# Kernel optimization log

Measured on AMD Instinct MI355X. Metric: run time of the kernel, lower is better.

Reference implementation:

```python
import jax, jax.numpy as jnp
import numpy as np

N_NODES = 100000
N_EDGES = 3200000
N_GRAPHS = 5000
IN_DIM = 11 + 3  # QM9 num_features + pos
HID = 64


def setup_inputs() -> dict:
    key = jax.random.key(0)
    ks = jax.random.split(key, 12)
    x = jax.random.normal(ks[0], (N_NODES, 11), dtype=jnp.float32)
    pos = jax.random.normal(ks[1], (N_NODES, 3), dtype=jnp.float32)
    edge_index = jax.random.randint(ks[2], (2, N_EDGES), 0, N_NODES, dtype=jnp.int32)
    batch = jnp.sort(jax.random.randint(ks[3], (N_NODES,), 0, N_GRAPHS, dtype=jnp.int32))
    s1 = 1.0 / np.sqrt(IN_DIM)
    s2 = 1.0 / np.sqrt(HID)
    return {
        'x': x,
        'pos': pos,
        'edge_index': edge_index,
        'batch': batch,
        'W1_l': jax.random.uniform(ks[4], (IN_DIM, HID), jnp.float32, -s1, s1),
        'W1_r': jax.random.uniform(ks[5], (IN_DIM, HID), jnp.float32, -s1, s1),
        'b1': jax.random.uniform(ks[6], (HID,), jnp.float32, -s1, s1),
        'W2_l': jax.random.uniform(ks[7], (HID, HID), jnp.float32, -s2, s2),
        'W2_r': jax.random.uniform(ks[8], (HID, HID), jnp.float32, -s2, s2),
        'b2': jax.random.uniform(ks[9], (HID,), jnp.float32, -s2, s2),
        'W_lin': jax.random.uniform(ks[10], (HID, 1), jnp.float32, -s2, s2),
        'b_lin': jax.random.uniform(ks[11], (1,), jnp.float32, -s2, s2),
    }


def _sage_conv(h, src, dst, W_l, W_r, b):
    # mean-aggregate source features at target nodes (PyG SAGEConv default)
    msg = h[src]  # [E, D] gather
    agg = jax.ops.segment_sum(msg, dst, num_segments=N_NODES)
    deg = jax.ops.segment_sum(jnp.ones((src.shape[0],), h.dtype), dst, num_segments=N_NODES)
    agg = agg / jnp.maximum(deg, 1.0)[:, None]
    return agg @ W_l + h @ W_r + b


def reference(x, pos, edge_index, batch, W1_l, W1_r, b1, W2_l, W2_r, b2, W_lin, b_lin):
    h = jnp.concatenate([x, pos], axis=1)  # [N, 14]
    src, dst = edge_index[0], edge_index[1]
    h = jax.nn.relu(_sage_conv(h, src, dst, W1_l, W1_r, b1))
    h = jax.nn.relu(_sage_conv(h, src, dst, W2_l, W2_r, b2))
    # global mean pool over graphs
    pooled = jax.ops.segment_sum(h, batch, num_segments=N_GRAPHS)
    cnt = jax.ops.segment_sum(jnp.ones((N_NODES,), h.dtype), batch, num_segments=N_GRAPHS)
    pooled = pooled / jnp.maximum(cnt, 1.0)[:, None]
    return pooled @ W_lin + b_lin  # [G, 1]
```

## Files before the change

kernel.cpp:

```cpp
#include <hip/hip_runtime.h>

#define IND 14
#define INDP 16
#define HIDD 64
#define RB 512
#define NB_MAX 256
#define BH_BLOCKS 512
#define CAP 18432

typedef unsigned int uint;
typedef unsigned short ushort;

__device__ __forceinline__ float bf16lo(uint u) { return __uint_as_float(u << 16); }
__device__ __forceinline__ float bf16hi(uint u) { return __uint_as_float(u & 0xFFFF0000u); }
__device__ __forceinline__ ushort f2bf(float f) {
    uint u = __float_as_uint(f);
    u += 0x7FFFu + ((u >> 16) & 1u);
    return (ushort)(u >> 16);
}

__global__ void build_h0p(const float* __restrict__ x, const float* __restrict__ pos,
                          float* __restrict__ h0p, ushort* __restrict__ h0h, int N) {
    int tid = blockIdx.x * blockDim.x + threadIdx.x;
    int total = N * INDP;
    if (tid >= total) return;
    int n = tid >> 4, d = tid & 15;
    float v = 0.0f;
    if (d < 11) v = x[n * 11 + d];
    else if (d < 14) v = pos[n * 3 + (d - 11)];
    h0p[tid] = v;
    h0h[tid] = f2bf(v);
}

__global__ __launch_bounds__(256) void bscat_fused(const int* __restrict__ ei,
                                                   int* __restrict__ gcur,
                                                   uint* __restrict__ pairs,
                                                   int E, int NB, int chunk) {
    __shared__ int cntS[NB_MAX];
    __shared__ int baseS[NB_MAX];
    cntS[threadIdx.x] = 0;
    __syncthreads();
    int start = blockIdx.x * chunk;
    int end = min(start + chunk, E);
    for (int e = start + threadIdx.x; e < end; e += 256)
        atomicAdd(&cntS[ei[E + e] >> 9], 1);
    __syncthreads();
    if (threadIdx.x < NB) {
        int c = cntS[threadIdx.x];
        baseS[threadIdx.x] = c ? atomicAdd(&gcur[threadIdx.x], c) : 0;
        cntS[threadIdx.x] = 0;
    }
    __syncthreads();
    for (int e = start + threadIdx.x; e < end; e += 256) {
        int s = ei[e], d = ei[E + e];
        int b = d >> 9;
        int p = atomicAdd(&cntS[b], 1) + baseS[b];
        pairs[(size_t)b * CAP + p] = ((uint)(d & (RB - 1)) << 17) | (uint)s;
    }
}

__global__ __launch_bounds__(1024) void csr_build(const uint* __restrict__ pairs,
                                                  const int* __restrict__ gcur,
                                                  int2* __restrict__ rowseg,
                                                  int* __restrict__ csr, int N) {
    __shared__ int s[RB];
    __shared__ int fillS[RB];
    int b = blockIdx.x;
    int cnt = gcur[b];
    size_t base = (size_t)b * CAP;
    int t = threadIdx.x;
    if (t < RB) { s[t] = 0; fillS[t] = 0; }
    __syncthreads();
    for (int i = t; i < cnt; i += 1024)
        atomicAdd(&s[pairs[base + i] >> 17], 1);
    __syncthreads();
    for (int off = 1; off < RB; off <<= 1) {
        int v = 0;
        if (t < RB && t >= off) v = s[t - off];
        __syncthreads();
        if (t < RB) s[t] += v;
        __syncthreads();
    }
    int node0 = b << 9;
    if (t < RB) {
        int node = node0 + t;
        if (node < N)
            rowseg[node] = make_int2((int)base + (t ? s[t - 1] : 0), (int)base + s[t]);
    }
    __syncthreads();
    for (int i = t; i < cnt; i += 1024) {
        uint pk = pairs[base + i];
        int local = pk >> 17;
        int p = atomicAdd(&fillS[local], 1);
        int segbase = local ? s[local - 1] : 0;
        csr[base + segbase + p] = (int)(pk & 0x1FFFFu);
    }
}

__global__ __launch_bounds__(512) void agg_layer1(
        const float* __restrict__ h0p, const ushort* __restrict__ h0h,
        const int2* __restrict__ rowseg, const int* __restrict__ csr,
        const float* __restrict__ W_l, const float* __restrict__ W_r,
        const float* __restrict__ b, float* __restrict__ h1f,
        ushort* __restrict__ h1h, int N) {
    __shared__ float sWl[IND * HIDD];
    __shared__ float sWr[IND * HIDD];
    __shared__ float sA[8][INDP];
    __shared__ float sS[8][INDP];
    for (int i = threadIdx.x; i < IND * HIDD; i += 512) {
        sWl[i] = W_l[i];
        sWr[i] = W_r[i];
    }
    int w = threadIdx.x >> 6, t = threadIdx.x & 63;
    int node = blockIdx.x * 8 + w;
    if (node < N) {
        int2 seg = rowseg[node];
        int beg = seg.x, end = seg.y;
        int s = t >> 1, hf = t & 1;
        float acc[8] = {0.f, 0.f, 0.f, 0.f, 0.f, 0.f, 0.f, 0.f};
        for (int cb = beg; cb < end; cb += 64) {
            int e0 = cb + s, e1 = e0 + 32;
            int i0 = csr[min(e0, end - 1)];
            int i1 = csr[min(e1, end - 1)];
            float m0 = (e0 < end) ? 1.f : 0.f;
            float m1 = (e1 < end) ? 1.f : 0.f;
            const uint4 v0 = *(const uint4*)(h0h + (size_t)i0 * INDP + hf * 8);
            const uint4 v1 = *(const uint4*)(h0h + (size_t)i1 * INDP + hf * 8);
            acc[0] = fmaf(m0, bf16lo(v0.x), acc[0]); acc[1] = fmaf(m0, bf16hi(v0.x), acc[1]);
            acc[2] = fmaf(m0, bf16lo(v0.y), acc[2]); acc[3] = fmaf(m0, bf16hi(v0.y), acc[3]);
            acc[4] = fmaf(m0, bf16lo(v0.z), acc[4]); acc[5] = fmaf(m0, bf16hi(v0.z), acc[5]);
            acc[6] = fmaf(m0, bf16lo(v0.w), acc[6]); acc[7] = fmaf(m0, bf16hi(v0.w), acc[7]);
            acc[0] = fmaf(m1, bf16lo(v1.x), acc[0]); acc[1] = fmaf(m1, bf16hi(v1.x), acc[1]);
            acc[2] = fmaf(m1, bf16lo(v1.y), acc[2]); acc[3] = fmaf(m1, bf16hi(v1.y), acc[3]);
            acc[4] = fmaf(m1, bf16lo(v1.z), acc[4]); acc[5] = fmaf(m1, bf16hi(v1.z), acc[5]);
            acc[6] = fmaf(m1, bf16lo(v1.w), acc[6]); acc[7] = fmaf(m1, bf16hi(v1.w), acc[7]);
        }
#pragma unroll
        for (int m = 2; m < 64; m <<= 1) {
#pragma unroll
            for (int j = 0; j < 8; ++j) acc[j] += __shfl_xor(acc[j], m, 64);
        }
        float invd = 1.0f / fmaxf((float)(end - beg), 1.0f);
        if (t < 2) {
#pragma unroll
            for (int j = 0; j < 8; ++j) sA[w][t * 8 + j] = acc[j] * invd;
        }
        if (t < INDP) sS[w][t] = h0p[(size_t)node * INDP + t];
    }
    __syncthreads();
    if (node >= N) return;
    float acc = b[t];
#pragma unroll
    for (int k = 0; k < IND; ++k)
        acc += sA[w][k] * sWl[k * HIDD + t] + sS[w][k] * sWr[k * HIDD + t];
    float val = fmaxf(acc, 0.0f);
    h1f[(size_t)node * HIDD + t] = val;
    h1h[(size_t)node * HIDD + t] = f2bf(val);
}

__global__ __launch_bounds__(512) void agg_layer2(
        const float* __restrict__ h1f, const ushort* __restrict__ h1h,
        const int2* __restrict__ rowseg, const int* __restrict__ csr,
        const int* __restrict__ batch,
        const float* __restrict__ W_l, const float* __restrict__ W_r,
        const float* __restrict__ b,
        float* __restrict__ pooled, float* __restrict__ cnt, int N) {
    __shared__ float sWl[HIDD * HIDD];
    __shared__ float sWr[HIDD * HIDD];
    __shared__ float sA[8][HIDD];
    __shared__ float sS[8][HIDD];
    for (int i = threadIdx.x; i < HIDD * HIDD; i += 512) {
        sWl[i] = W_l[i];
        sWr[i] = W_r[i];
    }
    int w = threadIdx.x >> 6, t = threadIdx.x & 63;
    int node = blockIdx.x * 8 + w;
    if (node < N) {
        int2 seg = rowseg[node];
        int beg = seg.x, end = seg.y;
        int s = t >> 3, p = t & 7;
        float acc[8] = {0.f, 0.f, 0.f, 0.f, 0.f, 0.f, 0.f, 0.f};
        for (int cb = beg; cb < end; cb += 32) {
            int e0 = cb + s, e1 = e0 + 8, e2 = e0 + 16, e3 = e0 + 24;
            int i0 = csr[min(e0, end - 1)];
            int i1 = csr[min(e1, end - 1)];
            int i2 = csr[min(e2, end - 1)];
            int i3 = csr[min(e3, end - 1)];
            float m0 = (e0 < end) ? 1.f : 0.f;
            float m1 = (e1 < end) ? 1.f : 0.f;
            float m2 = (e2 < end) ? 1.f : 0.f;
            float m3 = (e3 < end) ? 1.f : 0.f;
            const uint4 v0 = *(const uint4*)(h1h + (size_t)i0 * HIDD + p * 8);
            const uint4 v1 = *(const uint4*)(h1h + (size_t)i1 * HIDD + p * 8);
            const uint4 v2 = *(const uint4*)(h1h + (size_t)i2 * HIDD + p * 8);
            const uint4 v3 = *(const uint4*)(h1h + (size_t)i3 * HIDD + p * 8);
            acc[0] = fmaf(m0, bf16lo(v0.x), acc[0]); acc[1] = fmaf(m0, bf16hi(v0.x), acc[1]);
            acc[2] = fmaf(m0, bf16lo(v0.y), acc[2]); acc[3] = fmaf(m0, bf16hi(v0.y), acc[3]);
            acc[4] = fmaf(m0, bf16lo(v0.z), acc[4]); acc[5] = fmaf(m0, bf16hi(v0.z), acc[5]);
            acc[6] = fmaf(m0, bf16lo(v0.w), acc[6]); acc[7] = fmaf(m0, bf16hi(v0.w), acc[7]);
            acc[0] = fmaf(m1, bf16lo(v1.x), acc[0]); acc[1] = fmaf(m1, bf16hi(v1.x), acc[1]);
            acc[2] = fmaf(m1, bf16lo(v1.y), acc[2]); acc[3] = fmaf(m1, bf16hi(v1.y), acc[3]);
            acc[4] = fmaf(m1, bf16lo(v1.z), acc[4]); acc[5] = fmaf(m1, bf16hi(v1.z), acc[5]);
            acc[6] = fmaf(m1, bf16lo(v1.w), acc[6]); acc[7] = fmaf(m1, bf16hi(v1.w), acc[7]);
            acc[0] = fmaf(m2, bf16lo(v2.x), acc[0]); acc[1] = fmaf(m2, bf16hi(v2.x), acc[1]);
            acc[2] = fmaf(m2, bf16lo(v2.y), acc[2]); acc[3] = fmaf(m2, bf16hi(v2.y), acc[3]);
            acc[4] = fmaf(m2, bf16lo(v2.z), acc[4]); acc[5] = fmaf(m2, bf16hi(v2.z), acc[5]);
            acc[6] = fmaf(m2, bf16lo(v2.w), acc[6]); acc[7] = fmaf(m2, bf16hi(v2.w), acc[7]);
            acc[0] = fmaf(m3, bf16lo(v3.x), acc[0]); acc[1] = fmaf(m3, bf16hi(v3.x), acc[1]);
            acc[2] = fmaf(m3, bf16lo(v3.y), acc[2]); acc[3] = fmaf(m3, bf16hi(v3.y), acc[3]);
            acc[4] = fmaf(m3, bf16lo(v3.z), acc[4]); acc[5] = fmaf(m3, bf16hi(v3.z), acc[5]);
            acc[6] = fmaf(m3, bf16lo(v3.w), acc[6]); acc[7] = fmaf(m3, bf16hi(v3.w), acc[7]);
        }
#pragma unroll
        for (int m = 8; m < 64; m <<= 1) {
#pragma unroll
            for (int j = 0; j < 8; ++j) acc[j] += __shfl_xor(acc[j], m, 64);
        }
        float invd = 1.0f / fmaxf((float)(end - beg), 1.0f);
        if (t < 8) {
#pragma unroll
            for (int j = 0; j < 8; ++j) sA[w][t * 8 + j] = acc[j] * invd;
        }
        sS[w][t] = h1f[(size_t)node * HIDD + t];
    }
    __syncthreads();
    if (node >= N) return;
    float acc = b[t];
#pragma unroll 8
    for (int k = 0; k < HIDD; ++k)
        acc += sA[w][k] * sWl[k * HIDD + t] + sS[w][k] * sWr[k * HIDD + t];
    float val = fmaxf(acc, 0.0f);
    int g = batch[node];
    atomicAdd(pooled + (size_t)g * HIDD + t, val);
    if (t == 0) atomicAdd(cnt + g, 1.0f);
}

__global__ void final_k(const float* __restrict__ pooled, const float* __restrict__ cnt,
                        const float* __restrict__ W, const float* __restrict__ bl,
                        float* __restrict__ out, int G) {
    int g = blockIdx.x;
    if (g >= G) return;
    int t = threadIdx.x;
    float invc = 1.0f / fmaxf(cnt[g], 1.0f);
    float v = pooled[(size_t)g * HIDD + t] * invc * W[t];
#pragma unroll
    for (int o = 32; o > 0; o >>= 1) v += __shfl_down(v, o, 64);
    if (t == 0) out[g] = v + bl[0];
}

extern "C" void kernel_launch(void* const* d_in, const int* in_sizes, int n_in,
                              void* d_out, int out_size, void* d_ws, size_t ws_size,
                              hipStream_t stream) {
    const float* x   = (const float*)d_in[0];
    const float* pos = (const float*)d_in[1];
    const int* ei    = (const int*)d_in[2];
    const int* batch = (const int*)d_in[3];
    const float* W1l = (const float*)d_in[4];
    const float* W1r = (const float*)d_in[5];
    const float* b1  = (const float*)d_in[6];
    const float* W2l = (const float*)d_in[7];
    const float* W2r = (const float*)d_in[8];
    const float* b2  = (const float*)d_in[9];
    const float* Wl  = (const float*)d_in[10];
    const float* bl  = (const float*)d_in[11];
    float* out = (float*)d_out;

    int N = in_sizes[3];
    int E = in_sizes[2] / 2;
    int G = out_size;
    int NB = (N + RB - 1) >> 9;
    int chunk = (E + BH_BLOCKS - 1) / BH_BLOCKS;

    char* ws = (char*)d_ws;
    size_t off = 0;
    float* cnt = (float*)(ws + off);    off += (size_t)G * 4;
    float* pooled = (float*)(ws + off); off += (size_t)G * HIDD * 4;
    int* gcur = (int*)(ws + off);       off += (size_t)NB_MAX * 4;
    size_t zero_bytes = off;
    off = (off + 255) & ~(size_t)255;
    int2* rowseg = (int2*)(ws + off);   off += (size_t)N * 8;
    uint* pairs = (uint*)(ws + off);    off += (size_t)NB * CAP * 4;
    int* csr    = (int*)(ws + off);     off += (size_t)NB * CAP * 4;
    off = (off + 255) & ~(size_t)255;
    float* h0p  = (float*)(ws + off);   off += (size_t)N * INDP * 4;
    off = (off + 255) & ~(size_t)255;
    ushort* h0h = (ushort*)(ws + off);  off += (size_t)N * INDP * 2;
    off = (off + 255) & ~(size_t)255;
    float* h1f  = (float*)(ws + off);   off += (size_t)N * HIDD * 4;
    off = (off + 255) & ~(size_t)255;
    ushort* h1h = (ushort*)(ws + off);  off += (size_t)N * HIDD * 2;

    hipMemsetAsync(d_ws, 0, zero_bytes, stream);

    int blk = 256;
    build_h0p<<<((size_t)N * INDP + blk - 1) / blk, blk, 0, stream>>>(x, pos, h0p, h0h, N);
    bscat_fused<<<BH_BLOCKS, 256, 0, stream>>>(ei, gcur, pairs, E, NB, chunk);
    csr_build<<<NB, 1024, 0, stream>>>(pairs, gcur, rowseg, csr, N);
    agg_layer1<<<(N + 7) / 8, 512, 0, stream>>>(h0p, h0h, rowseg, csr, W1l, W1r, b1,
                                                h1f, h1h, N);
    agg_layer2<<<(N + 7) / 8, 512, 0, stream>>>(h1f, h1h, rowseg, csr, batch,
                                                W2l, W2r, b2, pooled, cnt, N);
    final_k<<<G, 64, 0, stream>>>(pooled, cnt, Wl, bl, out, G);
}
```

Baseline: 365.0 us.

## Split layer-2 dense matmul across warps by K and cache dst indices in LDS

In the layer-2 kernel, each wave now owns an 8-row slice of the weight matrices, keeps that slice in registers, and computes partial dot products for all 8 nodes in the block. The partials go to a shared buffer and are summed per node. This is meant to cut the repeated LDS weight reads in the per-node 64-step loop, at the cost of an extra barrier and 16KB more shared memory. Separately, the edge-bucketing kernel caches destination indices in LDS so the second pass does not re-read them from global memory. Layer 1's shared row stride is also padded from 16 to 20 floats, likely to reduce bank conflicts.

```diff
diff --git a/kernel.cpp b/kernel.cpp
--- a/kernel.cpp
+++ b/kernel.cpp
@@ -7,6 +7,8 @@
 #define NB_MAX 256
 #define BH_BLOCKS 512
 #define CAP 18432
+#define ROW1 20
+#define DSTS 6400
 
 typedef unsigned int uint;
 typedef unsigned short ushort;
@@ -38,12 +40,17 @@
                                                    int E, int NB, int chunk) {
     __shared__ int cntS[NB_MAX];
     __shared__ int baseS[NB_MAX];
+    __shared__ int dstS[DSTS];
     cntS[threadIdx.x] = 0;
     __syncthreads();
     int start = blockIdx.x * chunk;
     int end = min(start + chunk, E);
-    for (int e = start + threadIdx.x; e < end; e += 256)
-        atomicAdd(&cntS[ei[E + e] >> 9], 1);
+    int it = 0;
+    for (int e = start + threadIdx.x; e < end; e += 256, ++it) {
+        int d = ei[E + e];
+        dstS[it * 256 + threadIdx.x] = d;
+        atomicAdd(&cntS[d >> 9], 1);
+    }
     __syncthreads();
     if (threadIdx.x < NB) {
         int c = cntS[threadIdx.x];
@@ -51,8 +58,10 @@
         cntS[threadIdx.x] = 0;
     }
     __syncthreads();
-    for (int e = start + threadIdx.x; e < end; e += 256) {
-        int s = ei[e], d = ei[E + e];
+    it = 0;
+    for (int e = start + threadIdx.x; e < end; e += 256, ++it) {
+        int s = ei[e];
+        int d = dstS[it * 256 + threadIdx.x];
         int b = d >> 9;
         int p = atomicAdd(&cntS[b], 1) + baseS[b];
         pairs[(size_t)b * CAP + p] = ((uint)(d & (RB - 1)) << 17) | (uint)s;
@@ -105,8 +114,8 @@
         ushort* __restrict__ h1h, int N) {
     __shared__ float sWl[IND * HIDD];
     __shared__ float sWr[IND * HIDD];
-    __shared__ float sA[8][INDP];
-    __shared__ float sS[8][INDP];
+    __shared__ float sA[8][ROW1];
+    __shared__ float sS[8][ROW1];
     for (int i = threadIdx.x; i < IND * HIDD; i += 512) {
         sWl[i] = W_l[i];
         sWr[i] = W_r[i];
@@ -169,6 +178,7 @@
     __shared__ float sWr[HIDD * HIDD];
     __shared__ float sA[8][HIDD];
     __shared__ float sS[8][HIDD];
+    __shared__ float sP[8][8][HIDD];
     for (int i = threadIdx.x; i < HIDD * HIDD; i += 512) {
         sWl[i] = W_l[i];
         sWr[i] = W_r[i];
@@ -224,12 +234,33 @@
         sS[w][t] = h1f[(size_t)node * HIDD + t];
     }
     __syncthreads();
+    {
+        int kb = w * 8;
+        float wl[8], wr[8];
+#pragma unroll
+        for (int kk = 0; kk < 8; ++kk) {
+            wl[kk] = sWl[(kb + kk) * HIDD + t];
+            wr[kk] = sWr[(kb + kk) * HIDD + t];
+        }
+#pragma unroll
+        for (int n = 0; n < 8; ++n) {
+            const float4* pa = (const float4*)(&sA[n][kb]);
+            const float4* ps = (const float4*)(&sS[n][kb]);
+            float4 a0 = pa[0], a1 = pa[1], s0 = ps[0], s1 = ps[1];
+            float acc;
+            acc  = a0.x * wl[0] + a0.y * wl[1] + a0.z * wl[2] + a0.w * wl[3];
+            acc += a1.x * wl[4] + a1.y * wl[5] + a1.z * wl[6] + a1.w * wl[7];
+            acc += s0.x * wr[0] + s0.y * wr[1] + s0.z * wr[2] + s0.w * wr[3];
+            acc += s1.x * wr[4] + s1.y * wr[5] + s1.z * wr[6] + s1.w * wr[7];
+            sP[w][n][t] = acc;
+        }
+    }
+    __syncthreads();
     if (node >= N) return;
-    float acc = b[t];
-#pragma unroll 8
-    for (int k = 0; k < HIDD; ++k)
-        acc += sA[w][k] * sWl[k * HIDD + t] + sS[w][k] * sWr[k * HIDD + t];
-    float val = fmaxf(acc, 0.0f);
+    float v = b[t];
+#pragma unroll
+    for (int j = 0; j < 8; ++j) v += sP[j][w][t];
+    float val = fmaxf(v, 0.0f);
     int g = batch[node];
     atomicAdd(pooled + (size_t)g * HIDD + t, val);
     if (t == 0) atomicAdd(cnt + g, 1.0f);
```

Result: no change. 361.6 us (-0.9%).
